# Kernel optimization log

Measured on AMD Instinct MI355X. Metric: run time of the kernel, lower is better.

## Reference

```python
import jax, jax.numpy as jnp
import numpy as np

B, C, F, H = 16384, 64, 128, 128  # batch, conv1d_out_channel, in_features, hidden


def setup_inputs() -> dict:
    key = jax.random.key(0)
    k_x, k_w1, k_w2 = jax.random.split(key, 3)
    inputline = jax.random.normal(k_x, (B, C, F), dtype=jnp.float32)
    # Per-channel cloned Flowconf MLP params: Linear(F,H) -> ReLU -> Linear(H,1)
    W1 = jax.random.normal(k_w1, (C, F, H), dtype=jnp.float32) * (1.0 / np.sqrt(F))
    b1 = jnp.zeros((C, H), dtype=jnp.float32)
    W2 = jax.random.normal(k_w2, (C, H), dtype=jnp.float32) * (1.0 / np.sqrt(H))
    b2 = jnp.zeros((C,), dtype=jnp.float32)
    return {"inputline": inputline, "W1": W1, "b1": b1, "W2": W2, "b2": b2}


def reference(inputline, W1, b1, W2, b2) -> jnp.ndarray:
    # Batched over channels: replaces the Python loop over C cloned submodules
    # with indexed assignment into output[:, i].
    h = jax.nn.relu(jnp.einsum("bcf,cfh->bch", inputline, W1) + b1)  # [B,C,H]
    out = jnp.einsum("bch,ch->bc", h, W2) + b2                        # [B,C]
    return out.sum(axis=-1)                                           # [B]
```

## Files before the change

kernel.cpp:

```cpp
#include <hip/hip_runtime.h>
#include <hip/hip_bf16.h>

#define B_TOT 16384
#define C_CH  64
#define F_IN  128
#define H_HID 128
#define CG    4
#define TROWS 16
#define NSUB  64
#define ROWS  (NSUB * TROWS)

using f32x4  = __attribute__((ext_vector_type(4))) float;
using bf16x8 = __attribute__((ext_vector_type(8))) short;

__device__ inline unsigned pack2(float a, float b) {
    unsigned short lo = __builtin_bit_cast(unsigned short, __float2bfloat16(a));
    unsigned short hi = __builtin_bit_cast(unsigned short, __float2bfloat16(b));
    return (unsigned)lo | ((unsigned)hi << 16);
}

__device__ inline void gld_lds16(const float* g, float* l) {
    __builtin_amdgcn_global_load_lds(
        (const __attribute__((address_space(1))) void*)g,
        (__attribute__((address_space(3))) void*)l, 16, 0, 0);
}

__device__ inline void issue_tile(const float* __restrict__ X, size_t base0,
                                  int wave, int lane, float* buf) {
    #pragma unroll
    for (int q = 0; q < 2; ++q) {
        const int r = wave * 2 + q;
        const float* rowp = X + base0 + (size_t)r * (C_CH * F_IN);
        const int sw = r & 7;
        #pragma unroll
        for (int h = 0; h < 2; ++h)
            gld_lds16(rowp + h * 256 + ((lane ^ sw) << 2),
                      buf + r * 512 + h * 256);
    }
}

template<int N>
__device__ inline float compute_round(const float* __restrict__ xb,
                                      const bf16x8 (&wf)[4][4],
                                      const f32x4 (&w2c)[4],
                                      const f32x4 (&b1c)[4],
                                      int l15, int lg, int ch)
{
    asm volatile("s_waitcnt vmcnt(%0)" :: "i"(N) : "memory");
    __builtin_amdgcn_s_barrier();

    f32x4 acc[4];
    #pragma unroll
    for (int nf = 0; nf < 4; ++nf) acc[nf] = b1c[nf];

    const int sw = l15 & 7;
    const int rb = l15 * 512 + (ch >> 1) * 256;
    #pragma unroll
    for (int ks = 0; ks < 4; ++ks) {
        const int u = (ch & 1) * 32 + ks * 8 + lg * 2;
        float4 r0 = *reinterpret_cast<const float4*>(xb + rb + ((u ^ sw) << 2));
        float4 r1 = *reinterpret_cast<const float4*>(xb + rb + (((u + 1) ^ sw) << 2));
        uint4 px;
        px.x = pack2(r0.x, r0.y);
        px.y = pack2(r0.z, r0.w);
        px.z = pack2(r1.x, r1.y);
        px.w = pack2(r1.z, r1.w);
        bf16x8 xfrag = __builtin_bit_cast(bf16x8, px);
        #pragma unroll
        for (int nf = 0; nf < 4; ++nf)
            acc[nf] = __builtin_amdgcn_mfma_f32_16x16x32_bf16(
                wf[nf][ks], xfrag, acc[nf], 0, 0, 0);
    }

    float val = 0.f;
    #pragma unroll
    for (int nf = 0; nf < 4; ++nf)
        #pragma unroll
        for (int j = 0; j < 4; ++j)
            val += fmaxf(acc[nf][j], 0.f) * w2c[nf][j];
    val += __shfl_xor(val, 16, 64);
    val += __shfl_xor(val, 32, 64);
    return val;
}

__global__ __launch_bounds__(512, 2)
void fused_mlp_kernel(const float* __restrict__ X,
                      const float* __restrict__ W1,
                      const float* __restrict__ b1,
                      const float* __restrict__ W2,
                      const float* __restrict__ b2,
                      float* __restrict__ out)
{
    __shared__ alignas(16) float Xs[4 * TROWS * 512];

    const int t    = threadIdx.x;
    const int lane = t & 63;
    const int wave = t >> 6;
    const int l15  = lane & 15;
    const int lg   = lane >> 4;
    const int ch   = wave & 3;
    const int hh   = wave >> 2;

    const int c0 = blockIdx.x * CG;
    const int c  = c0 + ch;
    const int m0 = blockIdx.y * ROWS;

    float* bu0 = Xs;
    float* bu1 = Xs + TROWS * 512;
    float* bu2 = Xs + 2 * TROWS * 512;
    float* bu3 = Xs + 3 * TROWS * 512;

    const size_t cbase = ((size_t)m0 * C_CH + c0) * F_IN;
    const size_t tstep = (size_t)TROWS * C_CH * F_IN;
    issue_tile(X, cbase, wave, lane, bu0);
    issue_tile(X, cbase + tstep, wave, lane, bu1);
    issue_tile(X, cbase + 2 * tstep, wave, lane, bu2);

    bf16x8 wf[4][4];
    {
        const float* wb = W1 + (size_t)c * F_IN * H_HID + hh * 64 + l15;
        #pragma unroll
        for (int nf = 0; nf < 4; ++nf)
            #pragma unroll
            for (int ks = 0; ks < 4; ++ks) {
                const int f0 = ks * 32 + lg * 8;
                float v[8];
                #pragma unroll
                for (int e = 0; e < 8; ++e)
                    v[e] = wb[(size_t)(f0 + e) * H_HID + nf * 16];
                uint4 p;
                p.x = pack2(v[0], v[1]);
                p.y = pack2(v[2], v[3]);
                p.z = pack2(v[4], v[5]);
                p.w = pack2(v[6], v[7]);
                wf[nf][ks] = __builtin_bit_cast(bf16x8, p);
            }
    }
    f32x4 w2c[4], b1c[4];
    #pragma unroll
    for (int nf = 0; nf < 4; ++nf) {
        const int ho = c * H_HID + hh * 64 + nf * 16 + lg * 4;
        w2c[nf] = *reinterpret_cast<const f32x4*>(W2 + ho);
        b1c[nf] = *reinterpret_cast<const f32x4*>(b1 + ho);
    }
    const float b2c = (hh == 0) ? b2[c] : 0.f;

    #define DO_ROUND(NWAIT, SC, ISSUE)                                          \
        {                                                                       \
            float val = compute_round<NWAIT>(bu0, wf, w2c, b1c, l15, lg, ch);   \
            if (ISSUE)                                                          \
                issue_tile(X, cbase + (size_t)((SC) + 3) * tstep, wave, lane, bu3); \
            if (lane < 16) atomicAdd(&out[m0 + (SC) * TROWS + lane], val + b2c); \
            float* tmp = bu0; bu0 = bu1; bu1 = bu2; bu2 = bu3; bu3 = tmp;       \
        }

    DO_ROUND(8, 0, true)
    DO_ROUND(9, 1, true)
    DO_ROUND(10, 2, true)
    #pragma unroll 1
    for (int sc = 3; sc <= 61; ++sc)
        DO_ROUND(11, sc, (sc + 3 < NSUB))
    DO_ROUND(7, 62, false)
    DO_ROUND(3, 63, false)
    #undef DO_ROUND
}

extern "C" void kernel_launch(void* const* d_in, const int* in_sizes, int n_in,
                              void* d_out, int out_size, void* d_ws, size_t ws_size,
                              hipStream_t stream) {
    const float* X  = (const float*)d_in[0];
    const float* W1 = (const float*)d_in[1];
    const float* b1 = (const float*)d_in[2];
    const float* W2 = (const float*)d_in[3];
    const float* b2 = (const float*)d_in[4];
    float* out = (float*)d_out;

    hipMemsetAsync(out, 0, (size_t)out_size * sizeof(float), stream);

    dim3 grid(C_CH / CG, B_TOT / ROWS);
    fused_mlp_kernel<<<grid, dim3(512), 0, stream>>>(X, W1, b1, W2, b2, out);
}
```

Measured before the change: 106.4 us.

## Replace cross-block output atomics with per-group partial buffers and reduce kernel

Each channel-group block now atomically adds into its own slice of a workspace buffer rather than into the shared output. A separate kernel then sums the 16 partial slices into the final output, which removes atomic contention across channel groups. The LDS ring also shrinks from four to three buffers, so prefetch depth drops from three tiles to two, with the wait counts adjusted to match. The trade is an extra kernel launch, a larger memset and reduced latency hiding on the main X stream.

```diff
diff --git a/kernel.cpp b/kernel.cpp
--- a/kernel.cpp
+++ b/kernel.cpp
@@ -9,6 +9,7 @@
 #define TROWS 16
 #define NSUB  64
 #define ROWS  (NSUB * TROWS)
+#define NCG   (C_CH / CG)
 
 using f32x4  = __attribute__((ext_vector_type(4))) float;
 using bf16x8 = __attribute__((ext_vector_type(8))) short;
@@ -37,6 +38,7 @@
             gld_lds16(rowp + h * 256 + ((lane ^ sw) << 2),
                       buf + r * 512 + h * 256);
     }
+    asm volatile("" ::: "memory");
 }
 
 template<int N>
@@ -48,6 +50,7 @@
 {
     asm volatile("s_waitcnt vmcnt(%0)" :: "i"(N) : "memory");
     __builtin_amdgcn_s_barrier();
+    asm volatile("" ::: "memory");
 
     f32x4 acc[4];
     #pragma unroll
@@ -89,9 +92,10 @@
                       const float* __restrict__ b1,
                       const float* __restrict__ W2,
                       const float* __restrict__ b2,
-                      float* __restrict__ out)
+                      float* __restrict__ dest,
+                      int sstride)
 {
-    __shared__ alignas(16) float Xs[4 * TROWS * 512];
+    __shared__ alignas(16) float Xs[3 * TROWS * 512];
 
     const int t    = threadIdx.x;
     const int lane = t & 63;
@@ -104,17 +108,16 @@
     const int c0 = blockIdx.x * CG;
     const int c  = c0 + ch;
     const int m0 = blockIdx.y * ROWS;
+    const int dbase = blockIdx.x * sstride + m0;
 
     float* bu0 = Xs;
     float* bu1 = Xs + TROWS * 512;
     float* bu2 = Xs + 2 * TROWS * 512;
-    float* bu3 = Xs + 3 * TROWS * 512;
 
     const size_t cbase = ((size_t)m0 * C_CH + c0) * F_IN;
     const size_t tstep = (size_t)TROWS * C_CH * F_IN;
     issue_tile(X, cbase, wave, lane, bu0);
     issue_tile(X, cbase + tstep, wave, lane, bu1);
-    issue_tile(X, cbase + 2 * tstep, wave, lane, bu2);
 
     bf16x8 wf[4][4];
     {
@@ -149,20 +152,32 @@
         {                                                                       \
             float val = compute_round<NWAIT>(bu0, wf, w2c, b1c, l15, lg, ch);   \
             if (ISSUE)                                                          \
-                issue_tile(X, cbase + (size_t)((SC) + 3) * tstep, wave, lane, bu3); \
-            if (lane < 16) atomicAdd(&out[m0 + (SC) * TROWS + lane], val + b2c); \
-            float* tmp = bu0; bu0 = bu1; bu1 = bu2; bu2 = bu3; bu3 = tmp;       \
+                issue_tile(X, cbase + (size_t)((SC) + 2) * tstep, wave, lane, bu2); \
+            if (lane < 16) atomicAdd(&dest[dbase + (SC) * TROWS + lane], val + b2c); \
+            asm volatile("" ::: "memory");                                      \
+            float* tmp = bu0; bu0 = bu1; bu1 = bu2; bu2 = tmp;                  \
         }
 
-    DO_ROUND(8, 0, true)
-    DO_ROUND(9, 1, true)
-    DO_ROUND(10, 2, true)
+    DO_ROUND(4, 0, true)
+    DO_ROUND(5, 1, true)
     #pragma unroll 1
-    for (int sc = 3; sc <= 61; ++sc)
-        DO_ROUND(11, sc, (sc + 3 < NSUB))
-    DO_ROUND(7, 62, false)
-    DO_ROUND(3, 63, false)
+    for (int sc = 2; sc <= 62; ++sc)
+        DO_ROUND(6, sc, (sc + 2 < NSUB))
+    DO_ROUND(2, 63, false)
     #undef DO_ROUND
+}
+
+__global__ __launch_bounds__(256)
+void reduce_kernel(const float* __restrict__ part, float* __restrict__ out)
+{
+    const int idx = blockIdx.x * blockDim.x + threadIdx.x;
+    if (idx < B_TOT / 4) {
+        f32x4 acc = f32x4{0.f, 0.f, 0.f, 0.f};
+        #pragma unroll
+        for (int s = 0; s < NCG; ++s)
+            acc += *reinterpret_cast<const f32x4*>(part + (size_t)s * B_TOT + idx * 4);
+        *reinterpret_cast<f32x4*>(out + idx * 4) = acc;
+    }
 }
 
 extern "C" void kernel_launch(void* const* d_in, const int* in_sizes, int n_in,
@@ -175,8 +190,18 @@
     const float* b2 = (const float*)d_in[4];
     float* out = (float*)d_out;
 
-    hipMemsetAsync(out, 0, (size_t)out_size * sizeof(float), stream);
-
+    const size_t part_bytes = (size_t)NCG * B_TOT * sizeof(float);
     dim3 grid(C_CH / CG, B_TOT / ROWS);
-    fused_mlp_kernel<<<grid, dim3(512), 0, stream>>>(X, W1, b1, W2, b2, out);
-}
+
+    if (ws_size >= part_bytes) {
+        float* part = (float*)d_ws;
+        hipMemsetAsync(part, 0, part_bytes, stream);
+        fused_mlp_kernel<<<grid, dim3(512), 0, stream>>>(X, W1, b1, W2, b2,
+                                                         part, B_TOT);
+        reduce_kernel<<<dim3(B_TOT / 4 / 256), dim3(256), 0, stream>>>(part, out);
+    } else {
+        hipMemsetAsync(out, 0, (size_t)out_size * sizeof(float), stream);
+        fused_mlp_kernel<<<grid, dim3(512), 0, stream>>>(X, W1, b1, W2, b2,
+                                                         out, 0);
+    }
+}
```

Result: no change. 106.7 us (+0.4%).
